# Kernel tuning notes

Measured on AMD Instinct MI355X. Metric: run time of the kernel, lower is better.

## Reference

```python
import jax, jax.numpy as jnp
import numpy as np

MAX_N = 32        # mixture degree N
N_PTS = 16384     # number of scalar inputs
INIT_DECAY = 1.0


def setup_inputs() -> dict:
    key = jax.random.key(0)
    k1, _ = jax.random.split(key)
    # inputs assumed elementwise in [-1, 1]
    xs = jax.random.uniform(k1, (N_PTS,), dtype=jnp.float32, minval=-1.0, maxval=1.0)
    # learned logits param, init logits[n] = -n * init_decay (as in __init__)
    logits = -INIT_DECAY * jnp.arange(MAX_N + 1, dtype=jnp.float32)
    return {"xs": xs, "logits": logits}


def _psi(xs, logits, max_n):
    """psi(x) = concat_n sqrt(w_n) * phi_n(x); shape (P, 2*max_n+1).

    phi_0 = [1]; phi_n = [T_n(x), sqrt(1-x^2) * U_{n-1}(x)] for n>=1.
    Single linear-pass recurrence instead of per-degree recompute.
    """
    w = jax.nn.softmax(logits)          # (max_n+1,)
    sw = jnp.sqrt(w)
    xc = jnp.clip(xs, -1.0, 1.0)        # (P,)
    s = jnp.sqrt(jnp.clip(1.0 - xc * xc, 0.0))
    P = xs.shape[0]

    # T_0..T_max_n and U_0..U_max_n via one shared recurrence (fixed small loop)
    Ts = [jnp.ones_like(xc), xc]
    Us = [jnp.ones_like(xc), 2.0 * xc]
    for _ in range(2, max_n + 1):
        Ts.append(2.0 * xc * Ts[-1] - Ts[-2])
        Us.append(2.0 * xc * Us[-1] - Us[-2])
    T = jnp.stack(Ts, axis=-1)          # (P, max_n+1)
    U = jnp.stack(Us, axis=-1)          # (P, max_n+1)

    Tn = T[:, 1:]                       # T_1..T_N            (P, max_n)
    Un = U[:, :max_n]                   # U_0..U_{N-1}        (P, max_n)
    # interleave per degree: [T_n, s * U_{n-1}], weighted by sqrt(w_n)
    pair = jnp.stack([Tn, s[:, None] * Un], axis=-1)   # (P, max_n, 2)
    pair = pair * sw[1:][None, :, None]
    head = sw[0] * jnp.ones((P, 1), dtype=xs.dtype)    # sqrt(w_0) * phi_0
    return jnp.concatenate([head, pair.reshape(P, 2 * max_n)], axis=-1)


def reference(xs, logits):
    """gram(xs) = psi(xs) @ psi(xs)^T, shape (P, P)."""
    psi = _psi(xs, logits, MAX_N)       # (P, 2*MAX_N+1)
    return psi @ psi.T
```

## Files before the change

kernel.cpp:

```cpp
#include <hip/hip_runtime.h>
#include <hip/hip_bf16.h>
#include <math.h>

#define MAXN    32
#define NPTS    16384
#define RSTRIDE 64
#define BTA     64
#define BTB     256
#define NCHUNK  ((BTA + BTB) * RSTRIDE * 2 / 1024)
#define W0_OFF  (NPTS * RSTRIDE)

typedef __attribute__((ext_vector_type(8))) short         bf16x8;
typedef __attribute__((ext_vector_type(4))) float         f32x4;
typedef __attribute__((ext_vector_type(4))) unsigned int  u32x4;

__device__ inline ushort f2bf(float f) {
    union { float f; unsigned u; } v; v.f = f;
    unsigned u = v.u;
    u += 0x7FFFu + ((u >> 16) & 1u);
    return (ushort)(u >> 16);
}

__global__ __launch_bounds__(256) void psi_kernel(
    const float* __restrict__ xs, const float* __restrict__ logits,
    ushort* __restrict__ psi, float* __restrict__ w0scr)
{
    __shared__ ushort srow[256 * RSTRIDE];

    const int tid = threadIdx.x;
    const int pt  = blockIdx.x * 256 + tid;

    float x = xs[pt];
    x = fminf(1.0f, fmaxf(-1.0f, x));
    float s = sqrtf(fmaxf(0.0f, 1.0f - x * x));

    float m = -3.4e38f;
    #pragma unroll
    for (int n = 0; n <= MAXN; ++n) m = fmaxf(m, logits[n]);
    float sum = 0.0f;
    #pragma unroll
    for (int n = 0; n <= MAXN; ++n) sum += __expf(logits[n] - m);
    float inv = 1.0f / sum;

    if (pt == 0) w0scr[0] = __expf(logits[0] - m) * inv;

    ushort tmp[RSTRIDE];
    float Tm1 = 1.0f, T = x;
    float Um1 = 1.0f, U = 2.0f * x;
    float tx = 2.0f * x;
    #pragma unroll
    for (int n = 1; n <= MAXN; ++n) {
        float swn = sqrtf(__expf(logits[n] - m) * inv);
        tmp[2 * n - 2] = f2bf(swn * T);
        tmp[2 * n - 1] = f2bf(swn * (s * Um1));
        float Tn = tx * T - Tm1; Tm1 = T; T = Tn;
        float Un = tx * U - Um1; Um1 = U; U = Un;
    }

    {
        u32x4* lrow = (u32x4*)(srow + tid * RSTRIDE);
        const u32x4* src = (const u32x4*)tmp;
        const int rx = tid & 7;
        #pragma unroll
        for (int j = 0; j < 8; ++j) lrow[j ^ rx] = src[j];
    }
    __syncthreads();

    {
        const u32x4* ls = (const u32x4*)srow;
        u32x4* gd = (u32x4*)(psi + (size_t)blockIdx.x * 256 * RSTRIDE);
        #pragma unroll
        for (int i = 0; i < 8; ++i) gd[i * 256 + tid] = ls[i * 256 + tid];
    }
}

__device__ inline void load_lds16(const void* g, void* l) {
    __builtin_amdgcn_global_load_lds(
        (const __attribute__((address_space(1))) unsigned*)g,
        (__attribute__((address_space(3))) unsigned*)l, 16, 0, 0);
}

__global__ __launch_bounds__(256) void gram_kernel(
    const ushort* __restrict__ psi, const float* __restrict__ w0scr,
    float* __restrict__ out)
{
    __shared__ float ldsF[BTA * BTB];

    const int tid  = threadIdx.x;
    const int w    = tid >> 6;
    const int lane = tid & 63;
    const int bi   = blockIdx.y;
    const int bj   = blockIdx.x;

    const float w0 = w0scr[0];

    {
        const char* gA = (const char*)(psi + (size_t)bi * BTA * RSTRIDE);
        const char* gB = (const char*)(psi + (size_t)bj * BTB * RSTRIDE);
        char* lbase = (char*)ldsF;
        for (int q = w; q < NCHUNK; q += 4) {
            const char* src = (q < 8) ? (gA + q * 1024) : (gB + (q - 8) * 1024);
            load_lds16(src + lane * 16, lbase + q * 1024);
        }
    }
    __syncthreads();

    const int lr = lane & 15;
    const int lh = lane >> 4;
    const int cq = lh * 4;

    const char* aRow   = (const char*)ldsF + (w * 16 + lr) * 128;
    const char* bPanel = (const char*)ldsF + 8192;

    f32x4 acc[16];
    #pragma unroll
    for (int ct = 0; ct < 16; ++ct) acc[ct] = (f32x4){w0, w0, w0, w0};

    #pragma unroll
    for (int ks = 0; ks < 2; ++ks) {
        const int sx = ((ks * 4 + lh) ^ (lr & 7)) * 16;
        bf16x8 a = *(const bf16x8*)(aRow + sx);
        #pragma unroll
        for (int ct = 0; ct < 16; ++ct) {
            bf16x8 b = *(const bf16x8*)(bPanel + (ct * 16 + lr) * 128 + sx);
            acc[ct] = __builtin_amdgcn_mfma_f32_16x16x32_bf16(b, a, acc[ct], 0, 0, 0);
        }
    }

    __syncthreads();
    {
        const int row = w * 16 + lr;
        const int rxe = (row & 7) << 2;
        #pragma unroll
        for (int ct = 0; ct < 16; ++ct) {
            int col = (cq + ct * 16) ^ rxe;
            *(f32x4*)(ldsF + row * BTB + col) = acc[ct];
        }
    }
    __syncthreads();

    {
        #pragma unroll
        for (int p = 0; p < 16; ++p) {
            int row  = p * 4 + w;
            int colr = (lane * 4) ^ ((row & 7) << 2);
            f32x4 v = *(const f32x4*)(ldsF + row * BTB + colr);
            float* dst = out + (size_t)(bi * BTA + row) * NPTS + (size_t)bj * BTB + lane * 4;
            *(f32x4*)dst = v;
        }
    }
}

extern "C" void kernel_launch(void* const* d_in, const int* in_sizes, int n_in,
                              void* d_out, int out_size, void* d_ws, size_t ws_size,
                              hipStream_t stream) {
    const float* xs     = (const float*)d_in[0];
    const float* logits = (const float*)d_in[1];
    float* out          = (float*)d_out;
    ushort* psi         = (ushort*)d_ws;
    float*  w0scr       = (float*)((char*)d_ws + (size_t)W0_OFF * 2);

    psi_kernel<<<NPTS / 256, 256, 0, stream>>>(xs, logits, psi, w0scr);

    dim3 grid(NPTS / BTB, NPTS / BTA);
    gram_kernel<<<grid, 256, 0, stream>>>(psi, w0scr, out);
}
```

Before: 184.9 us.

## Restructure gram kernel into row-strip blocks with direct global B loads

Each block now owns 16 output rows spanning all columns. The A fragment is held in registers and B rows are read straight from global (L2) instead of being staged through LDS with a block-wide barrier. Each wave loops over column strips and stages its own tile through a private LDS region for coalesced stores, so no block synchronisation is needed. The intent is fewer, longer-lived blocks with no __syncthreads stalls and less launch/setup overhead per tile. In exchange, global B traffic per block rises and each wave's work is serialised over 16 strips.

```diff
diff --git a/kernel.cpp b/kernel.cpp
--- a/kernel.cpp
+++ b/kernel.cpp
@@ -5,9 +5,8 @@
 #define MAXN    32
 #define NPTS    16384
 #define RSTRIDE 64
-#define BTA     64
-#define BTB     256
-#define NCHUNK  ((BTA + BTB) * RSTRIDE * 2 / 1024)
+#define BTA     16
+#define STRIPC  256
 #define W0_OFF  (NPTS * RSTRIDE)
 
 typedef __attribute__((ext_vector_type(8))) short         bf16x8;
@@ -74,78 +73,57 @@
     }
 }
 
-__device__ inline void load_lds16(const void* g, void* l) {
-    __builtin_amdgcn_global_load_lds(
-        (const __attribute__((address_space(1))) unsigned*)g,
-        (__attribute__((address_space(3))) unsigned*)l, 16, 0, 0);
-}
-
 __global__ __launch_bounds__(256) void gram_kernel(
     const ushort* __restrict__ psi, const float* __restrict__ w0scr,
     float* __restrict__ out)
 {
-    __shared__ float ldsF[BTA * BTB];
+    __shared__ float buf[4 * BTA * STRIPC];
 
     const int tid  = threadIdx.x;
     const int w    = tid >> 6;
     const int lane = tid & 63;
-    const int bi   = blockIdx.y;
-    const int bj   = blockIdx.x;
+    const int lr   = lane & 15;
+    const int lh   = lane >> 4;
+    const int r7   = lr & 7;
+    const int bi   = blockIdx.x;
 
     const float w0 = w0scr[0];
 
-    {
-        const char* gA = (const char*)(psi + (size_t)bi * BTA * RSTRIDE);
-        const char* gB = (const char*)(psi + (size_t)bj * BTB * RSTRIDE);
-        char* lbase = (char*)ldsF;
-        for (int q = w; q < NCHUNK; q += 4) {
-            const char* src = (q < 8) ? (gA + q * 1024) : (gB + (q - 8) * 1024);
-            load_lds16(src + lane * 16, lbase + q * 1024);
-        }
-    }
-    __syncthreads();
+    const ushort* aRow = psi + (size_t)(bi * BTA + lr) * RSTRIDE;
+    bf16x8 a0 = *(const bf16x8*)(aRow + ((lh ^ r7) * 8));
+    bf16x8 a1 = *(const bf16x8*)(aRow + (((4 + lh) ^ r7) * 8));
 
-    const int lr = lane & 15;
-    const int lh = lane >> 4;
-    const int cq = lh * 4;
+    float* mybuf = buf + w * BTA * STRIPC;
+    const int rxw = r7 << 2;
 
-    const char* aRow   = (const char*)ldsF + (w * 16 + lr) * 128;
-    const char* bPanel = (const char*)ldsF + 8192;
+    for (int s = 0; s < 16; ++s) {
+        const int colbase = (s * 4 + w) * STRIPC;
 
-    f32x4 acc[16];
-    #pragma unroll
-    for (int ct = 0; ct < 16; ++ct) acc[ct] = (f32x4){w0, w0, w0, w0};
+        f32x4 acc[16];
+        #pragma unroll
+        for (int ct = 0; ct < 16; ++ct) acc[ct] = (f32x4){w0, w0, w0, w0};
 
-    #pragma unroll
-    for (int ks = 0; ks < 2; ++ks) {
-        const int sx = ((ks * 4 + lh) ^ (lr & 7)) * 16;
-        bf16x8 a = *(const bf16x8*)(aRow + sx);
+        const ushort* bBase = psi + (size_t)colbase * RSTRIDE;
         #pragma unroll
         for (int ct = 0; ct < 16; ++ct) {
-            bf16x8 b = *(const bf16x8*)(bPanel + (ct * 16 + lr) * 128 + sx);
-            acc[ct] = __builtin_amdgcn_mfma_f32_16x16x32_bf16(b, a, acc[ct], 0, 0, 0);
+            const ushort* bRow = bBase + (ct * 16 + lr) * RSTRIDE;
+            bf16x8 b0 = *(const bf16x8*)(bRow + ((lh ^ r7) * 8));
+            bf16x8 b1 = *(const bf16x8*)(bRow + (((4 + lh) ^ r7) * 8));
+            acc[ct] = __builtin_amdgcn_mfma_f32_16x16x32_bf16(b0, a0, acc[ct], 0, 0, 0);
+            acc[ct] = __builtin_amdgcn_mfma_f32_16x16x32_bf16(b1, a1, acc[ct], 0, 0, 0);
         }
-    }
 
-    __syncthreads();
-    {
-        const int row = w * 16 + lr;
-        const int rxe = (row & 7) << 2;
         #pragma unroll
         for (int ct = 0; ct < 16; ++ct) {
-            int col = (cq + ct * 16) ^ rxe;
-            *(f32x4*)(ldsF + row * BTB + col) = acc[ct];
+            int col = (lh * 4 + ct * 16) ^ rxw;
+            *(f32x4*)(mybuf + lr * STRIPC + col) = acc[ct];
         }
-    }
-    __syncthreads();
 
-    {
         #pragma unroll
-        for (int p = 0; p < 16; ++p) {
-            int row  = p * 4 + w;
-            int colr = (lane * 4) ^ ((row & 7) << 2);
-            f32x4 v = *(const f32x4*)(ldsF + row * BTB + colr);
-            float* dst = out + (size_t)(bi * BTA + row) * NPTS + (size_t)bj * BTB + lane * 4;
+        for (int r = 0; r < 16; ++r) {
+            int colr = (lane * 4) ^ ((r & 7) << 2);
+            f32x4 v = *(const f32x4*)(mybuf + r * STRIPC + colr);
+            float* dst = out + (size_t)(bi * BTA + r) * NPTS + colbase + lane * 4;
             *(f32x4*)dst = v;
         }
     }
@@ -162,6 +140,5 @@
 
     psi_kernel<<<NPTS / 256, 256, 0, stream>>>(xs, logits, psi, w0scr);
 
-    dim3 grid(NPTS / BTB, NPTS / BTA);
-    gram_kernel<<<grid, 256, 0, stream>>>(psi, w0scr, out);
+    gram_kernel<<<NPTS / BTA, 256, 0, stream>>>(psi, w0scr, out);
 }
```

Result: slower. 238.3 us (+28.9%).

## Shrink gram row tile to 32 and split B panel across waves

Applied to the files above, without the earlier changes.

Halves the A-tile height to 32 rows and sizes LDS to the staged panels (36 KB instead of 64 KB), so more blocks can be resident per CU. Each wave now computes a 32x64 sub-tile (2x4 MFMA tiles) over its own slice of the B panel instead of 16x256. The goal is more occupancy and overlap of the output store traffic, which dominates this kernel. In exchange the grid doubles in blocks and the B panel is reloaded twice as often.

```diff
diff --git a/kernel.cpp b/kernel.cpp
--- a/kernel.cpp
+++ b/kernel.cpp
@@ -5,7 +5,7 @@
 #define MAXN    32
 #define NPTS    16384
 #define RSTRIDE 64
-#define BTA     64
+#define BTA     32
 #define BTB     256
 #define NCHUNK  ((BTA + BTB) * RSTRIDE * 2 / 1024)
 #define W0_OFF  (NPTS * RSTRIDE)
@@ -80,15 +80,18 @@
         (__attribute__((address_space(3))) unsigned*)l, 16, 0, 0);
 }
 
-__global__ __launch_bounds__(256) void gram_kernel(
+__global__ __launch_bounds__(256, 4) void gram_kernel(
     const ushort* __restrict__ psi, const float* __restrict__ w0scr,
     float* __restrict__ out)
 {
-    __shared__ float ldsF[BTA * BTB];
+    __shared__ float ldsF[NCHUNK * 256];
 
     const int tid  = threadIdx.x;
     const int w    = tid >> 6;
     const int lane = tid & 63;
+    const int lr   = lane & 15;
+    const int lh   = lane >> 4;
+    const int r7   = lr & 7;
     const int bi   = blockIdx.y;
     const int bj   = blockIdx.x;
 
@@ -99,49 +102,52 @@
         const char* gB = (const char*)(psi + (size_t)bj * BTB * RSTRIDE);
         char* lbase = (char*)ldsF;
         for (int q = w; q < NCHUNK; q += 4) {
-            const char* src = (q < 8) ? (gA + q * 1024) : (gB + (q - 8) * 1024);
+            const char* src = (q < 4) ? (gA + q * 1024) : (gB + (q - 4) * 1024);
             load_lds16(src + lane * 16, lbase + q * 1024);
         }
     }
     __syncthreads();
 
-    const int lr = lane & 15;
-    const int lh = lane >> 4;
-    const int cq = lh * 4;
+    const char* aPanel = (const char*)ldsF;
+    const char* bPanel = (const char*)ldsF + 4096;
 
-    const char* aRow   = (const char*)ldsF + (w * 16 + lr) * 128;
-    const char* bPanel = (const char*)ldsF + 8192;
-
-    f32x4 acc[16];
+    f32x4 acc[2][4];
     #pragma unroll
-    for (int ct = 0; ct < 16; ++ct) acc[ct] = (f32x4){w0, w0, w0, w0};
+    for (int rt = 0; rt < 2; ++rt)
+        #pragma unroll
+        for (int ct = 0; ct < 4; ++ct) acc[rt][ct] = (f32x4){w0, w0, w0, w0};
 
     #pragma unroll
     for (int ks = 0; ks < 2; ++ks) {
-        const int sx = ((ks * 4 + lh) ^ (lr & 7)) * 16;
-        bf16x8 a = *(const bf16x8*)(aRow + sx);
+        const int sx = ((ks * 4 + lh) ^ r7) * 16;
+        bf16x8 a0 = *(const bf16x8*)(aPanel + (lr      ) * 128 + sx);
+        bf16x8 a1 = *(const bf16x8*)(aPanel + (16 + lr ) * 128 + sx);
         #pragma unroll
-        for (int ct = 0; ct < 16; ++ct) {
-            bf16x8 b = *(const bf16x8*)(bPanel + (ct * 16 + lr) * 128 + sx);
-            acc[ct] = __builtin_amdgcn_mfma_f32_16x16x32_bf16(b, a, acc[ct], 0, 0, 0);
+        for (int ct = 0; ct < 4; ++ct) {
+            bf16x8 b = *(const bf16x8*)(bPanel + (w * 64 + ct * 16 + lr) * 128 + sx);
+            acc[0][ct] = __builtin_amdgcn_mfma_f32_16x16x32_bf16(b, a0, acc[0][ct], 0, 0, 0);
+            acc[1][ct] = __builtin_amdgcn_mfma_f32_16x16x32_bf16(b, a1, acc[1][ct], 0, 0, 0);
         }
     }
 
     __syncthreads();
     {
-        const int row = w * 16 + lr;
-        const int rxe = (row & 7) << 2;
         #pragma unroll
-        for (int ct = 0; ct < 16; ++ct) {
-            int col = (cq + ct * 16) ^ rxe;
-            *(f32x4*)(ldsF + row * BTB + col) = acc[ct];
+        for (int rt = 0; rt < 2; ++rt) {
+            const int row = rt * 16 + lr;
+            const int rxe = (row & 7) << 2;
+            #pragma unroll
+            for (int ct = 0; ct < 4; ++ct) {
+                int col = (w * 64 + ct * 16 + lh * 4) ^ rxe;
+                *(f32x4*)(ldsF + row * BTB + col) = acc[rt][ct];
+            }
         }
     }
     __syncthreads();
 
     {
         #pragma unroll
-        for (int p = 0; p < 16; ++p) {
+        for (int p = 0; p < 8; ++p) {
             int row  = p * 4 + w;
             int colr = (lane * 4) ^ ((row & 7) << 2);
             f32x4 v = *(const f32x4*)(ldsF + row * BTB + colr);
```

Result: no change. 182.4 us, median of 2 (-1.4%).
